# Optimization experiments

Hardware: AMD Instinct MI355X
Metric: run time of the kernel (lower is better)

Reference implementation:

```python
import jax, jax.numpy as jnp
import numpy as np

FEATURE_WEIGHTS = {"local": 0.4, "phrase": 0.4, "global": 0.2, "input": 0.1}
ADV_WEIGHTS = (0.4, 0.4, 0.2)  # stage_2 progressive weights
NOTE_OFF_START = 128
TIME_SHIFT_START = 256
VELOCITY_START = 768
EPS = 1e-12


def setup_inputs() -> dict:
    key = jax.random.key(0)
    ks = jax.random.split(key, 12)
    B, S, P, D = 32, 2048, 128, 512
    f = lambda k, shp: jax.random.normal(k, shp, dtype=jnp.float32)
    return {
        "real_local": f(ks[0], (B, S, D)),
        "real_phrase": f(ks[1], (B, P, D)),
        "real_global": f(ks[2], (B, D)),
        "real_input": f(ks[3], (B, S, D)),
        "fake_local": f(ks[4], (B, S, D)),
        "fake_phrase": f(ks[5], (B, P, D)),
        "fake_global": f(ks[6], (B, D)),
        "fake_input": f(ks[7], (B, S, D)),
        "local_logits": f(ks[8], (B, S)),
        "phrase_logits": f(ks[9], (B, P)),
        "global_logits": f(ks[10], (B, 1)),
        "tokens": jax.random.randint(ks[11], (B, S), 0, 774, dtype=jnp.int32),
    }


def _l2_normalize(x):
    # matches F.normalize(p=2, dim=-1): x / max(||x||, eps)
    n = jnp.sqrt(jnp.sum(x * x, axis=-1, keepdims=True))
    return x / jnp.maximum(n, EPS)


def _feature_matching(real_feats, fake_feats):
    total = 0.0
    for name, w in FEATURE_WEIGHTS.items():
        r = _l2_normalize(real_feats[name])
        f = _l2_normalize(fake_feats[name])
        diff = f.mean(axis=0) - jax.lax.stop_gradient(r.mean(axis=0))
        total = total + w * jnp.mean(diff * diff)
    return total / len(FEATURE_WEIGHTS)


def _musical_perceptual(tokens):
    B, S = tokens.shape
    # rhythm consistency
    time_shifts = ((tokens >= TIME_SHIFT_START) & (tokens < VELOCITY_START)).astype(jnp.float32)
    rhythm = jnp.mean(jnp.abs(jnp.diff(time_shifts, axis=1)))
    # harmonic coherence (vectorized form of the per-timestep python loop:
    # sum over i of batch-mean, then divide by seq_len)
    note_on = tokens < NOTE_OFF_START
    pitches = tokens * note_on.astype(tokens.dtype)
    pc = pitches % 12
    interval = jnp.abs(pc[:, :-1] - pc[:, 1:])
    harsh = ((interval == 6) | (interval == 11)).astype(jnp.float32)
    harmony = jnp.sum(jnp.mean(harsh, axis=0)) / S
    # melodic smoothness
    pdiff = jnp.diff(pitches.astype(jnp.float32), axis=1)
    melody = jnp.mean((jnp.abs(pdiff) > 12).astype(jnp.float32))
    return rhythm + harmony + melody


def _bce_with_logits_ones(logits):
    # BCEWithLogits(x, target=1) = softplus(-x)
    return jnp.mean(jax.nn.softplus(-logits))


def _adversarial(local_logits, phrase_logits, global_logits):
    w = ADV_WEIGHTS
    return (w[0] * _bce_with_logits_ones(local_logits)
            + w[1] * _bce_with_logits_ones(phrase_logits)
            + w[2] * _bce_with_logits_ones(global_logits))


def reference(real_local, real_phrase, real_global, real_input,
              fake_local, fake_phrase, fake_global, fake_input,
              local_logits, phrase_logits, global_logits, tokens):
    real_feats = {"local": real_local, "phrase": real_phrase,
                  "global": real_global, "input": real_input}
    fake_feats = {"local": fake_local, "phrase": fake_phrase,
                  "global": fake_global, "input": fake_input}
    fm = _feature_matching(real_feats, fake_feats)
    musical = _musical_perceptual(tokens)
    adv = _adversarial(local_logits, phrase_logits, global_logits)
    return fm + musical + adv
```

## Files before the change

### kernel.cpp

```cpp
#include <hip/hip_runtime.h>
#include <math.h>


#define B_ 32
#define S_ 2048
#define P_ 128
#define D_ 512

__global__ void zero_out_kernel(float* out) {
    if (threadIdx.x == 0 && blockIdx.x == 0) out[0] = 0.0f;
}

__global__ __launch_bounds__(256) void fm_kernel(
    const float* __restrict__ real_local, const float* __restrict__ real_phrase,
    const float* __restrict__ real_global, const float* __restrict__ real_input,
    const float* __restrict__ fake_local, const float* __restrict__ fake_phrase,
    const float* __restrict__ fake_global, const float* __restrict__ fake_input,
    float* __restrict__ out)
{
    const int NTASK = 2 * S_ + P_ + 1;
    int gtid = blockIdx.x * blockDim.x + threadIdx.x;
    int wave_id = gtid >> 6;
    int lane = threadIdx.x & 63;
    if (wave_id >= NTASK) return;

    const float* rp;
    const float* fp;
    long long base;
    long long rowStride;
    float scale;

    if (wave_id < S_) {
        int s = wave_id;
        rp = real_local; fp = fake_local;
        base = (long long)s * D_;
        rowStride = (long long)S_ * D_;
        scale = 0.4f / (4.0f * 1024.0f * (float)S_ * (float)D_);
    } else if (wave_id < 2 * S_) {
        int s = wave_id - S_;
        rp = real_input; fp = fake_input;
        base = (long long)s * D_;
        rowStride = (long long)S_ * D_;
        scale = 0.1f / (4.0f * 1024.0f * (float)S_ * (float)D_);
    } else if (wave_id < 2 * S_ + P_) {
        int p = wave_id - 2 * S_;
        rp = real_phrase; fp = fake_phrase;
        base = (long long)p * D_;
        rowStride = (long long)P_ * D_;
        scale = 0.4f / (4.0f * 1024.0f * (float)P_ * (float)D_);
    } else {
        rp = real_global; fp = fake_global;
        base = 0;
        rowStride = D_;
        scale = 0.2f / (4.0f * 1024.0f * (float)D_);
    }

    float4 a0 = {0.f, 0.f, 0.f, 0.f};
    float4 a1 = {0.f, 0.f, 0.f, 0.f};

    #pragma unroll 1
    for (int pass = 0; pass < 2; ++pass) {
        const float* ptr = pass ? fp : rp;
        const float sgn = pass ? 1.0f : -1.0f;
        #pragma unroll 1
        for (int b = 0; b < B_; ++b) {
            const float4* row = (const float4*)(ptr + base + (long long)b * rowStride);
            float4 x0 = row[lane];
            float4 x1 = row[64 + lane];
            float ss = x0.x * x0.x + x0.y * x0.y + x0.z * x0.z + x0.w * x0.w
                     + x1.x * x1.x + x1.y * x1.y + x1.z * x1.z + x1.w * x1.w;
            #pragma unroll
            for (int off = 32; off > 0; off >>= 1)
                ss += __shfl_xor(ss, off, 64);
            float inv = sgn / fmaxf(sqrtf(ss), 1e-12f);
            a0.x = fmaf(x0.x, inv, a0.x);
            a0.y = fmaf(x0.y, inv, a0.y);
            a0.z = fmaf(x0.z, inv, a0.z);
            a0.w = fmaf(x0.w, inv, a0.w);
            a1.x = fmaf(x1.x, inv, a1.x);
            a1.y = fmaf(x1.y, inv, a1.y);
            a1.z = fmaf(x1.z, inv, a1.z);
            a1.w = fmaf(x1.w, inv, a1.w);
        }
    }

    float ssum = a0.x * a0.x + a0.y * a0.y + a0.z * a0.z + a0.w * a0.w
               + a1.x * a1.x + a1.y * a1.y + a1.z * a1.z + a1.w * a1.w;
    #pragma unroll
    for (int off = 32; off > 0; off >>= 1)
        ssum += __shfl_xor(ssum, off, 64);

    if (lane == 0) atomicAdd(out, ssum * scale);
}

__device__ __forceinline__ float softplus_neg(float x) {
    float z = -x;
    return fmaxf(z, 0.0f) + log1pf(expf(-fabsf(z)));
}

__global__ __launch_bounds__(256) void small_kernel(
    const float* __restrict__ local_logits,
    const float* __restrict__ phrase_logits,
    const float* __restrict__ global_logits,
    const int* __restrict__ tokens,
    float* __restrict__ out)
{
    int gid = blockIdx.x * blockDim.x + threadIdx.x;
    float acc = 0.0f;

    const int NPAIR = B_ * (S_ - 1);
    if (gid < NPAIR) {
        int b = gid / (S_ - 1);
        int j = gid - b * (S_ - 1);
        int t0 = tokens[b * S_ + j];
        int t1 = tokens[b * S_ + j + 1];
        float ts0 = (t0 >= 256 && t0 < 768) ? 1.0f : 0.0f;
        float ts1 = (t1 >= 256 && t1 < 768) ? 1.0f : 0.0f;
        float rhythm = fabsf(ts1 - ts0);
        int p0 = (t0 < 128) ? t0 : 0;
        int p1 = (t1 < 128) ? t1 : 0;
        int pc0 = p0 % 12;
        int pc1 = p1 % 12;
        int iv = abs(pc0 - pc1);
        float harsh = (iv == 6 || iv == 11) ? 1.0f : 0.0f;
        int pd = p1 - p0;
        float mel = (abs(pd) > 12) ? 1.0f : 0.0f;
        acc += rhythm * (1.0f / (float)NPAIR)
             + harsh * (1.0f / ((float)B_ * (float)S_))
             + mel * (1.0f / (float)NPAIR);
    }

    if (gid < B_ * S_)   acc += 0.4f * softplus_neg(local_logits[gid])  / (float)(B_ * S_);
    if (gid < B_ * P_)   acc += 0.4f * softplus_neg(phrase_logits[gid]) / (float)(B_ * P_);
    if (gid < B_)        acc += 0.2f * softplus_neg(global_logits[gid]) / (float)B_;

    #pragma unroll
    for (int off = 32; off > 0; off >>= 1)
        acc += __shfl_xor(acc, off, 64);

    __shared__ float warp_sums[4];
    int wid = threadIdx.x >> 6;
    int lane = threadIdx.x & 63;
    if (lane == 0) warp_sums[wid] = acc;
    __syncthreads();
    if (threadIdx.x == 0) {
        float t = warp_sums[0] + warp_sums[1] + warp_sums[2] + warp_sums[3];
        atomicAdd(out, t);
    }
}

extern "C" void kernel_launch(void* const* d_in, const int* in_sizes, int n_in,
                              void* d_out, int out_size, void* d_ws, size_t ws_size,
                              hipStream_t stream) {
    const float* real_local   = (const float*)d_in[0];
    const float* real_phrase  = (const float*)d_in[1];
    const float* real_global  = (const float*)d_in[2];
    const float* real_input   = (const float*)d_in[3];
    const float* fake_local   = (const float*)d_in[4];
    const float* fake_phrase  = (const float*)d_in[5];
    const float* fake_global  = (const float*)d_in[6];
    const float* fake_input   = (const float*)d_in[7];
    const float* local_logits  = (const float*)d_in[8];
    const float* phrase_logits = (const float*)d_in[9];
    const float* global_logits = (const float*)d_in[10];
    const int*   tokens        = (const int*)d_in[11];
    float* out = (float*)d_out;

    zero_out_kernel<<<1, 64, 0, stream>>>(out);

    const int NTASK = 2 * S_ + P_ + 1;
    int fm_blocks = (NTASK * 64 + 255) / 256;
    fm_kernel<<<fm_blocks, 256, 0, stream>>>(
        real_local, real_phrase, real_global, real_input,
        fake_local, fake_phrase, fake_global, fake_input, out);

    small_kernel<<<(B_ * S_) / 256, 256, 0, stream>>>(
        local_logits, phrase_logits, global_logits, tokens, out);
}
```

Measured before the change: 486.3 us.

## Split each feature-matching column task across a full block of four waves

Each block now handles one sequence/phrase column instead of one wave per column. The 64 batch-pass rows are split across 4 waves and 4 row-groups per wave, with 16 lanes loading 8 float4 per row. Partial normalized sums are reduced via shuffles and shared memory before the squared-norm reduction. This raises memory-level parallelism and cuts serial loop length per wave, at the cost of more registers and extra shared-memory reduction and syncs.

```diff
diff --git a/kernel.cpp b/kernel.cpp
--- a/kernel.cpp
+++ b/kernel.cpp
@@ -6,6 +6,7 @@
 #define S_ 2048
 #define P_ 128
 #define D_ 512
+#define NTASK (2 * S_ + P_ + 1)
 
 __global__ void zero_out_kernel(float* out) {
     if (threadIdx.x == 0 && blockIdx.x == 0) out[0] = 0.0f;
@@ -18,79 +19,118 @@
     const float* __restrict__ fake_global, const float* __restrict__ fake_input,
     float* __restrict__ out)
 {
-    const int NTASK = 2 * S_ + P_ + 1;
-    int gtid = blockIdx.x * blockDim.x + threadIdx.x;
-    int wave_id = gtid >> 6;
-    int lane = threadIdx.x & 63;
-    if (wave_id >= NTASK) return;
-
-    const float* rp;
-    const float* fp;
-    long long base;
-    long long rowStride;
+    const int task = blockIdx.x;
+    const int part = threadIdx.x >> 6;
+    const int lane = threadIdx.x & 63;
+    const int r = lane >> 4;
+    const int c = lane & 15;
+
+    const float* rp; const float* fp;
+    long long base, rowStride;
     float scale;
-
-    if (wave_id < S_) {
-        int s = wave_id;
+    if (task < S_) {
         rp = real_local; fp = fake_local;
-        base = (long long)s * D_;
-        rowStride = (long long)S_ * D_;
+        base = (long long)task * D_; rowStride = (long long)S_ * D_;
         scale = 0.4f / (4.0f * 1024.0f * (float)S_ * (float)D_);
-    } else if (wave_id < 2 * S_) {
-        int s = wave_id - S_;
+    } else if (task < 2 * S_) {
+        int s = task - S_;
         rp = real_input; fp = fake_input;
-        base = (long long)s * D_;
-        rowStride = (long long)S_ * D_;
+        base = (long long)s * D_; rowStride = (long long)S_ * D_;
         scale = 0.1f / (4.0f * 1024.0f * (float)S_ * (float)D_);
-    } else if (wave_id < 2 * S_ + P_) {
-        int p = wave_id - 2 * S_;
+    } else if (task < 2 * S_ + P_) {
+        int p = task - 2 * S_;
         rp = real_phrase; fp = fake_phrase;
-        base = (long long)p * D_;
-        rowStride = (long long)P_ * D_;
+        base = (long long)p * D_; rowStride = (long long)P_ * D_;
         scale = 0.4f / (4.0f * 1024.0f * (float)P_ * (float)D_);
     } else {
         rp = real_global; fp = fake_global;
-        base = 0;
-        rowStride = D_;
+        base = 0; rowStride = D_;
         scale = 0.2f / (4.0f * 1024.0f * (float)D_);
     }
 
-    float4 a0 = {0.f, 0.f, 0.f, 0.f};
-    float4 a1 = {0.f, 0.f, 0.f, 0.f};
+    float4 acc[8];
+    #pragma unroll
+    for (int j = 0; j < 8; ++j) acc[j] = make_float4(0.f, 0.f, 0.f, 0.f);
 
     #pragma unroll 1
-    for (int pass = 0; pass < 2; ++pass) {
-        const float* ptr = pass ? fp : rp;
-        const float sgn = pass ? 1.0f : -1.0f;
-        #pragma unroll 1
-        for (int b = 0; b < B_; ++b) {
-            const float4* row = (const float4*)(ptr + base + (long long)b * rowStride);
-            float4 x0 = row[lane];
-            float4 x1 = row[64 + lane];
-            float ss = x0.x * x0.x + x0.y * x0.y + x0.z * x0.z + x0.w * x0.w
-                     + x1.x * x1.x + x1.y * x1.y + x1.z * x1.z + x1.w * x1.w;
-            #pragma unroll
-            for (int off = 32; off > 0; off >>= 1)
-                ss += __shfl_xor(ss, off, 64);
-            float inv = sgn / fmaxf(sqrtf(ss), 1e-12f);
-            a0.x = fmaf(x0.x, inv, a0.x);
-            a0.y = fmaf(x0.y, inv, a0.y);
-            a0.z = fmaf(x0.z, inv, a0.z);
-            a0.w = fmaf(x0.w, inv, a0.w);
-            a1.x = fmaf(x1.x, inv, a1.x);
-            a1.y = fmaf(x1.y, inv, a1.y);
-            a1.z = fmaf(x1.z, inv, a1.z);
-            a1.w = fmaf(x1.w, inv, a1.w);
+    for (int gi = 0; gi < 4; ++gi) {
+        int g = part * 4 + gi;
+        int combo = g * 4 + r;
+        int pass = combo >> 5;
+        int b = combo & 31;
+        const float4* row4 = (const float4*)((pass ? fp : rp) + base
+                              + (long long)b * rowStride);
+        float4 x[8];
+        #pragma unroll
+        for (int j = 0; j < 8; ++j) x[j] = row4[c + 16 * j];
+
+        float ss = 0.f;
+        #pragma unroll
+        for (int j = 0; j < 8; ++j)
+            ss += x[j].x * x[j].x + x[j].y * x[j].y
+                + x[j].z * x[j].z + x[j].w * x[j].w;
+        ss += __shfl_xor(ss, 1, 64);
+        ss += __shfl_xor(ss, 2, 64);
+        ss += __shfl_xor(ss, 4, 64);
+        ss += __shfl_xor(ss, 8, 64);
+
+        float inv = (pass ? 1.0f : -1.0f) / fmaxf(sqrtf(ss), 1e-12f);
+        #pragma unroll
+        for (int j = 0; j < 8; ++j) {
+            acc[j].x = fmaf(x[j].x, inv, acc[j].x);
+            acc[j].y = fmaf(x[j].y, inv, acc[j].y);
+            acc[j].z = fmaf(x[j].z, inv, acc[j].z);
+            acc[j].w = fmaf(x[j].w, inv, acc[j].w);
         }
     }
 
-    float ssum = a0.x * a0.x + a0.y * a0.y + a0.z * a0.z + a0.w * a0.w
-               + a1.x * a1.x + a1.y * a1.y + a1.z * a1.z + a1.w * a1.w;
+    #pragma unroll
+    for (int j = 0; j < 8; ++j) {
+        acc[j].x += __shfl_xor(acc[j].x, 16, 64);
+        acc[j].y += __shfl_xor(acc[j].y, 16, 64);
+        acc[j].z += __shfl_xor(acc[j].z, 16, 64);
+        acc[j].w += __shfl_xor(acc[j].w, 16, 64);
+        acc[j].x += __shfl_xor(acc[j].x, 32, 64);
+        acc[j].y += __shfl_xor(acc[j].y, 32, 64);
+        acc[j].z += __shfl_xor(acc[j].z, 32, 64);
+        acc[j].w += __shfl_xor(acc[j].w, 32, 64);
+    }
+
+    __shared__ float part_vec[4 * 512];
+    __shared__ float wave_sums[4];
+    float4* pv = (float4*)(part_vec + part * 512);
+    if (r == 0) {
+        pv[c]      = acc[0];
+        pv[16 + c] = acc[1];
+        pv[32 + c] = acc[2];
+        pv[48 + c] = acc[3];
+    } else if (r == 1) {
+        pv[64 + c]  = acc[4];
+        pv[80 + c]  = acc[5];
+        pv[96 + c]  = acc[6];
+        pv[112 + c] = acc[7];
+    }
+    __syncthreads();
+
+    const float2* pv2 = (const float2*)part_vec;
+    int tid = threadIdx.x;
+    float2 a0 = pv2[tid];
+    float2 a1 = pv2[256 + tid];
+    float2 a2 = pv2[512 + tid];
+    float2 a3 = pv2[768 + tid];
+    float v0 = a0.x + a1.x + a2.x + a3.x;
+    float v1 = a0.y + a1.y + a2.y + a3.y;
+    float ssq = v0 * v0 + v1 * v1;
+
     #pragma unroll
     for (int off = 32; off > 0; off >>= 1)
-        ssum += __shfl_xor(ssum, off, 64);
-
-    if (lane == 0) atomicAdd(out, ssum * scale);
+        ssq += __shfl_xor(ssq, off, 64);
+    if (lane == 0) wave_sums[part] = ssq;
+    __syncthreads();
+    if (tid == 0) {
+        float t = wave_sums[0] + wave_sums[1] + wave_sums[2] + wave_sums[3];
+        atomicAdd(out, t * scale);
+    }
 }
 
 __device__ __forceinline__ float softplus_neg(float x) {
@@ -119,12 +159,9 @@
         float rhythm = fabsf(ts1 - ts0);
         int p0 = (t0 < 128) ? t0 : 0;
         int p1 = (t1 < 128) ? t1 : 0;
-        int pc0 = p0 % 12;
-        int pc1 = p1 % 12;
-        int iv = abs(pc0 - pc1);
+        int iv = abs(p0 % 12 - p1 % 12);
         float harsh = (iv == 6 || iv == 11) ? 1.0f : 0.0f;
-        int pd = p1 - p0;
-        float mel = (abs(pd) > 12) ? 1.0f : 0.0f;
+        float mel = (abs(p1 - p0) > 12) ? 1.0f : 0.0f;
         acc += rhythm * (1.0f / (float)NPAIR)
              + harsh * (1.0f / ((float)B_ * (float)S_))
              + mel * (1.0f / (float)NPAIR);
@@ -168,9 +205,7 @@
 
     zero_out_kernel<<<1, 64, 0, stream>>>(out);
 
-    const int NTASK = 2 * S_ + P_ + 1;
-    int fm_blocks = (NTASK * 64 + 255) / 256;
-    fm_kernel<<<fm_blocks, 256, 0, stream>>>(
+    fm_kernel<<<NTASK, 256, 0, stream>>>(
         real_local, real_phrase, real_global, real_input,
         fake_local, fake_phrase, fake_global, fake_input, out);
 
```

Measured after the change: 465.9 us. -4.2%, faster.
